# Performance work log

Measured on AMD Instinct MI355X. Metric: run time of the kernel, lower is better.

Reference implementation:

```python
import jax, jax.numpy as jnp
import numpy as np

N_NODES = 50000
N_EDGES = 1600000
IN_DIM = 6
H = 64


def _sage_conv(x, src, dst, W_l, b_l, W_r, num_nodes):
    """PyG SAGEConv (aggr='mean'): out = lin_l(mean_{j in N(i)} x_j) + lin_r(x_i).
    lin_l has bias, lin_r has no bias (PyG default)."""
    # mean-aggregate neighbor features at destination nodes
    agg = jax.ops.segment_sum(x[src], dst, num_segments=num_nodes)          # [N, d]
    cnt = jax.ops.segment_sum(jnp.ones((src.shape[0],), x.dtype), dst,
                              num_segments=num_nodes)                        # [N]
    mean = agg / jnp.maximum(cnt, 1.0)[:, None]
    return mean @ W_l + b_l + x @ W_r


def setup_inputs() -> dict:
    key = jax.random.key(0)
    ks = jax.random.split(key, 8)
    x = jax.random.normal(ks[0], (N_NODES, IN_DIM), dtype=jnp.float32)
    edge_index = jax.random.randint(ks[1], (2, N_EDGES), 0, N_NODES, dtype=jnp.int64)
    # Kaiming-ish scaled params
    def lin(k, fan_in, fan_out):
        return jax.random.normal(k, (fan_in, fan_out), dtype=jnp.float32) / np.sqrt(fan_in)
    return {
        "x": x,
        "edge_index": edge_index,
        "W1_l": lin(ks[2], IN_DIM, H),
        "b1_l": jnp.zeros((H,), jnp.float32),
        "W1_r": lin(ks[3], IN_DIM, H),
        "W2_l": lin(ks[4], H, H),
        "b2_l": jnp.zeros((H,), jnp.float32),
        "W2_r": lin(ks[5], H, H),
    }


def reference(x, edge_index, W1_l, b1_l, W1_r, W2_l, b2_l, W2_r):
    src, dst = edge_index[0], edge_index[1]
    n = x.shape[0]
    z = jax.nn.relu(_sage_conv(x, src, dst, W1_l, b1_l, W1_r, n))  # [N, H]
    z = _sage_conv(z, src, dst, W2_l, b2_l, W2_r, n)               # [N, H]
    return z
```

## Files before the change

kernel.cpp:

```cpp
#include <hip/hip_runtime.h>

#define N_NODES 50000
#define N_EDGES 1600000
#define IN_DIM 6
#define H 64

#define NBUCKET 196
#define NBLK 196
#define EPB 8192
#define BCAP 9216

#define L2PAD 72
#define ZPLANE ((size_t)(N_NODES + 1) * 32)

__device__ __forceinline__ float bf2f(unsigned short u) {
    return __uint_as_float(((unsigned int)u) << 16);
}
__device__ __forceinline__ unsigned short f2bf(float f) {
    unsigned int u = __float_as_uint(f);
    u += 0x7fffu + ((u >> 16) & 1u);
    return (unsigned short)(u >> 16);
}

__global__ __launch_bounds__(512) void scatter_bucketed(
        const int* __restrict__ ei,
        const float* __restrict__ x,
        int* __restrict__ gcur,
        unsigned int* __restrict__ ebin,
        const float* __restrict__ W2l,
        const float* __restrict__ W2r,
        unsigned short* __restrict__ Wlt,
        unsigned short* __restrict__ Wrt,
        unsigned short* __restrict__ z,
        float* __restrict__ xp) {
    int t = threadIdx.x;
    int gid = blockIdx.x * 512 + t;
    if (gid < N_NODES) {
        const float2* xr = (const float2*)(x + (size_t)gid * IN_DIM);
        float2 p0 = xr[0], p1 = xr[1], p2 = xr[2];
        float4* xw = (float4*)(xp + ((size_t)gid << 3));
        xw[0] = make_float4(p0.x, p0.y, p1.x, p1.y);
        xw[1] = make_float4(p2.x, p2.y, 0.f, 0.f);
    }
    if (blockIdx.x == NBLK) {
        for (int i = t; i < H * H; i += 512) {
            int k = i >> 6, f = i & 63;
            Wlt[f * H + k] = f2bf(W2l[i]);
            Wrt[f * H + k] = f2bf(W2r[i]);
        }
        if (t < 64)
            z[(size_t)(t >> 5) * ZPLANE + (size_t)N_NODES * 32 + (t & 31)] = 0;
        return;
    }
    __shared__ unsigned int sedge[EPB];
    __shared__ int hist[NBUCKET];
    __shared__ int cur[NBUCKET];
    for (int i = t; i < NBUCKET; i += 512) hist[i] = 0;
    __syncthreads();
    int e0 = blockIdx.x * EPB;
    int cnt = min(EPB, N_EDGES - e0);
    const int4* s4 = (const int4*)(ei + e0);
    const int4* d4 = (const int4*)(ei + N_EDGES + e0);
    for (int k = t; k * 4 < cnt; k += 512) {
        int4 sv = s4[k];
        int4 dv = d4[k];
        sedge[k * 4 + 0] = ((unsigned)sv.x << 16) | (unsigned)dv.x;
        sedge[k * 4 + 1] = ((unsigned)sv.y << 16) | (unsigned)dv.y;
        sedge[k * 4 + 2] = ((unsigned)sv.z << 16) | (unsigned)dv.z;
        sedge[k * 4 + 3] = ((unsigned)sv.w << 16) | (unsigned)dv.w;
        atomicAdd(&hist[dv.x >> 8], 1);
        atomicAdd(&hist[dv.y >> 8], 1);
        atomicAdd(&hist[dv.z >> 8], 1);
        atomicAdd(&hist[dv.w >> 8], 1);
    }
    __syncthreads();
    for (int i = t; i < NBUCKET; i += 512)
        cur[i] = atomicAdd(&gcur[i], hist[i]);
    __syncthreads();
    for (int k = t; k * 4 < cnt; k += 512) {
#pragma unroll
        for (int j = 0; j < 4; j++) {
            unsigned int p = sedge[k * 4 + j];
            int b = (int)(p & 0xffffu) >> 8;
            int pos = atomicAdd(&cur[b], 1);
            if (pos < BCAP) ebin[(size_t)b * BCAP + pos] = p;
        }
    }
}

__global__ __launch_bounds__(1024) void bucket_layer1(
        const unsigned int* __restrict__ ebin,
        const int* __restrict__ gcur,
        const float* __restrict__ xp,
        const float* __restrict__ W1l,
        const float* __restrict__ b1,
        const float* __restrict__ W1r,
        int2* __restrict__ rowpair,
        unsigned short* __restrict__ esrc,
        unsigned short* __restrict__ z) {
    __shared__ int raw[BCAP];
    __shared__ unsigned short ssrc[BCAP];
    __shared__ int sdeg[256];
    __shared__ int sstart[256];
    __shared__ int scur[256];
    __shared__ int wsum[4];
    __shared__ float sW1l[IN_DIM * H];
    __shared__ float sW1r[IN_DIM * H];
    float* smx   = (float*)raw;
    float* spart = (float*)raw + 4096;

    int t = threadIdx.x;
    int lane = t & 63, w = t >> 6;
    int b = blockIdx.x;
    int base = b << 8;
    int nn = min(256, N_NODES - base);
    int ebase = b * BCAP;
    int cnt = min(gcur[b], BCAP);

    if (t < 256) sdeg[t] = 0;
    if (t < IN_DIM * H) { sW1l[t] = W1l[t]; sW1r[t] = W1r[t]; }
    for (int i = t; i < cnt; i += 1024) raw[i] = (int)ebin[ebase + i];
    __syncthreads();
    for (int i = t; i < cnt; i += 1024) atomicAdd(&sdeg[raw[i] & 0xff], 1);
    __syncthreads();
    int v = 0, s = 0;
    if (t < 256) {
        v = sdeg[t]; s = v;
#pragma unroll
        for (int off = 1; off < 64; off <<= 1) {
            int u = __shfl_up(s, off);
            if (lane >= off) s += u;
        }
        if (lane == 63) wsum[w] = s;
    }
    __syncthreads();
    if (t < 256) {
        int woff = 0;
        for (int k = 0; k < w; k++) woff += wsum[k];
        int excl = s - v + woff;
        sstart[t] = excl;
        scur[t] = excl;
        if (t < nn) rowpair[base + t] = make_int2(ebase + excl, ebase + excl + v);
    }
    __syncthreads();
    for (int i = t; i < cnt; i += 1024) {
        int p = raw[i];
        int pos = atomicAdd(&scur[p & 0xff], 1);
        ssrc[pos] = (unsigned short)((unsigned)p >> 16);
    }
    __syncthreads();
    for (int i = t; i < cnt; i += 1024)
        esrc[ebase + i] = ssrc[i];
    for (int i = t; i < nn * 8; i += 1024) {
        int node = i >> 3, k = i & 7;
        if (k < 6) smx[node * 16 + 6 + k] = xp[(size_t)(base + node) * 8 + k];
    }

    int node = t & 255, q = t >> 8;
    float a0 = 0.f, a1 = 0.f, a2 = 0.f, a3 = 0.f, a4 = 0.f, a5 = 0.f;
    int deg = 0, st = 0;
    if (node < nn) { deg = sdeg[node]; st = sstart[node]; }
    for (int i = st + q; i < st + deg; i += 4) {
        int src = ssrc[i];
        const float4* xs = (const float4*)(xp + ((size_t)src << 3));
        float4 p0 = xs[0], p1 = xs[1];
        a0 += p0.x; a1 += p0.y; a2 += p0.z;
        a3 += p0.w; a4 += p1.x; a5 += p1.y;
    }
    if (q > 0 && node < nn) {
        float* sp = &spart[(q - 1) * (256 * 6) + node * 6];
        sp[0] = a0; sp[1] = a1; sp[2] = a2; sp[3] = a3; sp[4] = a4; sp[5] = a5;
    }
    __syncthreads();
    if (q == 0 && node < nn) {
        float inv = 1.0f / fmaxf((float)deg, 1.0f);
        const float* p1p = &spart[0 * (256 * 6) + node * 6];
        const float* p2p = &spart[1 * (256 * 6) + node * 6];
        const float* p3p = &spart[2 * (256 * 6) + node * 6];
        smx[node * 16 + 0] = (a0 + p1p[0] + p2p[0] + p3p[0]) * inv;
        smx[node * 16 + 1] = (a1 + p1p[1] + p2p[1] + p3p[1]) * inv;
        smx[node * 16 + 2] = (a2 + p1p[2] + p2p[2] + p3p[2]) * inv;
        smx[node * 16 + 3] = (a3 + p1p[3] + p2p[3] + p3p[3]) * inv;
        smx[node * 16 + 4] = (a4 + p1p[4] + p2p[4] + p3p[4]) * inv;
        smx[node * 16 + 5] = (a5 + p1p[5] + p2p[5] + p3p[5]) * inv;
    }
    __syncthreads();

    int feat = t & 63, ng = t >> 6;
    float wl[IN_DIM], wr[IN_DIM];
#pragma unroll
    for (int k = 0; k < IN_DIM; k++) { wl[k] = sW1l[k * H + feat]; wr[k] = sW1r[k * H + feat]; }
    float bias = b1[feat];
    int plane = feat >> 5, f5 = feat & 31;
    unsigned short* zw = z + (size_t)plane * ZPLANE + f5;
    for (int nb = ng; nb < nn; nb += 16) {
        const float4* row = (const float4*)&smx[nb * 16];
        float4 r0 = row[0], r1 = row[1], r2 = row[2];
        float acc = bias;
        acc += r0.x * wl[0] + r0.y * wl[1] + r0.z * wl[2]
             + r0.w * wl[3] + r1.x * wl[4] + r1.y * wl[5];
        acc += r1.z * wr[0] + r1.w * wr[1] + r2.x * wr[2]
             + r2.y * wr[3] + r2.z * wr[4] + r2.w * wr[5];
        zw[(size_t)(base + nb) * 32] = f2bf(fmaxf(acc, 0.0f));
    }
}

__global__ __launch_bounds__(512) void layer2_mfma(
        const unsigned short* __restrict__ zin,
        const int2* __restrict__ rowpair,
        const unsigned short* __restrict__ esrc,
        const unsigned short* __restrict__ Wlt,
        const float* __restrict__ b2,
        const unsigned short* __restrict__ Wrt,
        float* __restrict__ out) {
    typedef short bf16x8 __attribute__((ext_vector_type(8)));
    typedef float f32x4 __attribute__((ext_vector_type(4)));
    __shared__ __attribute__((aligned(16))) unsigned short smean[32 * L2PAD];
    __shared__ __attribute__((aligned(16))) unsigned short szl[32 * L2PAD];
    __shared__ __attribute__((aligned(16))) unsigned short sWl[64 * L2PAD];
    __shared__ __attribute__((aligned(16))) unsigned short sWr[64 * L2PAD];

    int t = threadIdx.x;
    int w = t >> 6, lane = t & 63;
    int g8 = lane >> 3, l8 = lane & 7;
    int n0 = blockIdx.x * 32;

    {
        const ushort4* wl4 = (const ushort4*)Wlt;
        const ushort4* wr4 = (const ushort4*)Wrt;
        for (int qi = t; qi < H * H / 4; qi += 512) {
            int f = qi >> 4, kq = qi & 15;
            *(ushort4*)&sWl[f * L2PAD + kq * 4] = wl4[qi];
            *(ushort4*)&sWr[f * L2PAD + kq * 4] = wr4[qi];
        }
    }

#pragma unroll 1
    for (int pass = 0; pass < 2; pass++) {
        const unsigned short* zp = zin + (size_t)pass * ZPLANE;
        for (int q = 0; q < 4; q++) {
            int ln = w * 4 + q;
            int n = n0 + ln;
            bool valid = (n < N_NODES);
            int r0 = 0, r1 = 0;
            if (valid) { int2 rp = rowpair[n]; r0 = rp.x; r1 = rp.y; }
            float4 acc = make_float4(0.f, 0.f, 0.f, 0.f);
            for (int base = r0; base < r1; base += 64) {
                int ii = base + lane;
                int idx = (ii < r1) ? (int)esrc[ii] : N_NODES;
                int rem = r1 - base;
#pragma unroll
                for (int tt = 0; tt < 4; tt++) {
                    int s = __shfl(idx, tt * 8 + g8);
                    const ushort4* zr = (const ushort4*)(zp + (size_t)s * 32);
                    ushort4 vv = zr[l8];
                    acc.x += bf2f(vv.x); acc.y += bf2f(vv.y);
                    acc.z += bf2f(vv.z); acc.w += bf2f(vv.w);
                }
                if (rem > 32) {
#pragma unroll
                    for (int tt = 4; tt < 8; tt++) {
                        int s = __shfl(idx, tt * 8 + g8);
                        const ushort4* zr = (const ushort4*)(zp + (size_t)s * 32);
                        ushort4 vv = zr[l8];
                        acc.x += bf2f(vv.x); acc.y += bf2f(vv.y);
                        acc.z += bf2f(vv.z); acc.w += bf2f(vv.w);
                    }
                }
            }
#pragma unroll
            for (int off = 8; off < 64; off <<= 1) {
                acc.x += __shfl_xor(acc.x, off);
                acc.y += __shfl_xor(acc.y, off);
                acc.z += __shfl_xor(acc.z, off);
                acc.w += __shfl_xor(acc.w, off);
            }
            float inv = 1.0f / fmaxf((float)(r1 - r0), 1.0f);
            if (g8 == 0) {
                ushort4 mb;
                mb.x = f2bf(acc.x * inv); mb.y = f2bf(acc.y * inv);
                mb.z = f2bf(acc.z * inv); mb.w = f2bf(acc.w * inv);
                *(ushort4*)&smean[ln * L2PAD + pass * 32 + l8 * 4] = mb;
            }
            if (pass == 0) {
                int nz = valid ? n : N_NODES;
                szl[ln * L2PAD + lane] =
                    zin[(size_t)(lane >> 5) * ZPLANE + (size_t)nz * 32 + (lane & 31)];
            }
        }
    }
    __syncthreads();

    int g = lane >> 4, lg = lane & 15;
    int nb = w >> 2, fb = w & 3;
    f32x4 acc = {0.f, 0.f, 0.f, 0.f};
#pragma unroll
    for (int ks = 0; ks < 2; ks++) {
        int ko = ks * 32 + g * 8;
        bf16x8 aM = *(const bf16x8*)&smean[(nb * 16 + lg) * L2PAD + ko];
        bf16x8 aZ = *(const bf16x8*)&szl[(nb * 16 + lg) * L2PAD + ko];
        bf16x8 bL = *(const bf16x8*)&sWl[(fb * 16 + lg) * L2PAD + ko];
        bf16x8 bR = *(const bf16x8*)&sWr[(fb * 16 + lg) * L2PAD + ko];
        acc = __builtin_amdgcn_mfma_f32_16x16x32_bf16(aM, bL, acc, 0, 0, 0);
        acc = __builtin_amdgcn_mfma_f32_16x16x32_bf16(aZ, bR, acc, 0, 0, 0);
    }
    float bias = b2[fb * 16 + lg];
#pragma unroll
    for (int r = 0; r < 4; r++) {
        int node = n0 + nb * 16 + g * 4 + r;
        if (node < N_NODES)
            out[(size_t)node * H + fb * 16 + lg] = acc[r] + bias;
    }
}

extern "C" void kernel_launch(void* const* d_in, const int* in_sizes, int n_in,
                              void* d_out, int out_size, void* d_ws, size_t ws_size,
                              hipStream_t stream) {
    const float* x   = (const float*)d_in[0];
    const int*   ei  = (const int*)d_in[1];
    const float* W1l = (const float*)d_in[2];
    const float* b1  = (const float*)d_in[3];
    const float* W1r = (const float*)d_in[4];
    const float* W2l = (const float*)d_in[5];
    const float* b2  = (const float*)d_in[6];
    const float* W2r = (const float*)d_in[7];
    float* out = (float*)d_out;

    int* gcur = (int*)d_ws;
    int2* rowpair = (int2*)(gcur + 208);
    unsigned int*   ebin = (unsigned int*)(rowpair + N_NODES);
    unsigned short* esrc = (unsigned short*)(ebin + (size_t)NBUCKET * BCAP);
    unsigned short* z    = esrc + (size_t)NBUCKET * BCAP;
    unsigned short* Wlt  = z + 2 * ZPLANE;
    unsigned short* Wrt  = Wlt + H * H;
    float* xp = (float*)(Wrt + H * H);

    hipMemsetAsync(gcur, 0, NBUCKET * sizeof(int), stream);

    scatter_bucketed<<<NBLK + 1, 512, 0, stream>>>(ei, x, gcur, ebin,
                                                   W2l, W2r, Wlt, Wrt, z, xp);
    bucket_layer1<<<NBUCKET, 1024, 0, stream>>>(ebin, gcur, xp, W1l, b1, W1r,
                                                rowpair, esrc, z);
    layer2_mfma<<<(N_NODES + 31) / 32, 512, 0, stream>>>(z, rowpair, esrc,
                                                         Wlt, b2, Wrt, out);
}
```

Before: 154.3 us.

## Replace bucketed edge binning with global per-node degree count, scan, and atomic placement

The two-pass bucket scatter (LDS histogram plus bucket bins, then an in-block counting sort) is replaced by three simpler kernels. One counts per-node in-degree with global atomics, one computes per-bucket exclusive scans into CSR-like row ranges, and one places source indices with per-node global atomics. Layer 1 aggregation is rewritten as a wave-per-node gather with shuffle reduction over 32-node blocks. This removes the intermediate packed edge bin array and the large-LDS layer-1 kernel. In exchange it adds two kernel launches and heavy contended global atomics over 1.6M edges, and the neighbor order within each row becomes nondeterministic.

```diff
diff --git a/kernel.cpp b/kernel.cpp
--- a/kernel.cpp
+++ b/kernel.cpp
@@ -6,12 +6,12 @@
 #define H 64
 
 #define NBUCKET 196
-#define NBLK 196
-#define EPB 8192
 #define BCAP 9216
 
 #define L2PAD 72
 #define ZPLANE ((size_t)(N_NODES + 1) * 32)
+
+#define K1GRID 512
 
 __device__ __forceinline__ float bf2f(unsigned short u) {
     return __uint_as_float(((unsigned int)u) << 16);
@@ -22,11 +22,10 @@
     return (unsigned short)(u >> 16);
 }
 
-__global__ __launch_bounds__(512) void scatter_bucketed(
+__global__ __launch_bounds__(1024) void count_deg(
         const int* __restrict__ ei,
         const float* __restrict__ x,
-        int* __restrict__ gcur,
-        unsigned int* __restrict__ ebin,
+        int* __restrict__ deg,
         const float* __restrict__ W2l,
         const float* __restrict__ W2r,
         unsigned short* __restrict__ Wlt,
@@ -34,155 +33,148 @@
         unsigned short* __restrict__ z,
         float* __restrict__ xp) {
     int t = threadIdx.x;
-    int gid = blockIdx.x * 512 + t;
-    if (gid < N_NODES) {
-        const float2* xr = (const float2*)(x + (size_t)gid * IN_DIM);
+    int tid = blockIdx.x * 1024 + t;
+    if (tid < N_NODES) {
+        const float2* xr = (const float2*)(x + (size_t)tid * IN_DIM);
         float2 p0 = xr[0], p1 = xr[1], p2 = xr[2];
-        float4* xw = (float4*)(xp + ((size_t)gid << 3));
+        float4* xw = (float4*)(xp + ((size_t)tid << 3));
         xw[0] = make_float4(p0.x, p0.y, p1.x, p1.y);
         xw[1] = make_float4(p2.x, p2.y, 0.f, 0.f);
-    }
-    if (blockIdx.x == NBLK) {
-        for (int i = t; i < H * H; i += 512) {
+    } else if (tid == N_NODES) {
+        float4* xw = (float4*)(xp + ((size_t)N_NODES << 3));
+        xw[0] = make_float4(0.f, 0.f, 0.f, 0.f);
+        xw[1] = make_float4(0.f, 0.f, 0.f, 0.f);
+    }
+    if (blockIdx.x == K1GRID - 1) {
+        for (int i = t; i < H * H; i += 1024) {
             int k = i >> 6, f = i & 63;
             Wlt[f * H + k] = f2bf(W2l[i]);
             Wrt[f * H + k] = f2bf(W2r[i]);
         }
         if (t < 64)
             z[(size_t)(t >> 5) * ZPLANE + (size_t)N_NODES * 32 + (t & 31)] = 0;
-        return;
-    }
-    __shared__ unsigned int sedge[EPB];
-    __shared__ int hist[NBUCKET];
-    __shared__ int cur[NBUCKET];
-    for (int i = t; i < NBUCKET; i += 512) hist[i] = 0;
-    __syncthreads();
-    int e0 = blockIdx.x * EPB;
-    int cnt = min(EPB, N_EDGES - e0);
-    const int4* s4 = (const int4*)(ei + e0);
-    const int4* d4 = (const int4*)(ei + N_EDGES + e0);
-    for (int k = t; k * 4 < cnt; k += 512) {
-        int4 sv = s4[k];
-        int4 dv = d4[k];
-        sedge[k * 4 + 0] = ((unsigned)sv.x << 16) | (unsigned)dv.x;
-        sedge[k * 4 + 1] = ((unsigned)sv.y << 16) | (unsigned)dv.y;
-        sedge[k * 4 + 2] = ((unsigned)sv.z << 16) | (unsigned)dv.z;
-        sedge[k * 4 + 3] = ((unsigned)sv.w << 16) | (unsigned)dv.w;
-        atomicAdd(&hist[dv.x >> 8], 1);
-        atomicAdd(&hist[dv.y >> 8], 1);
-        atomicAdd(&hist[dv.z >> 8], 1);
-        atomicAdd(&hist[dv.w >> 8], 1);
-    }
-    __syncthreads();
-    for (int i = t; i < NBUCKET; i += 512)
-        cur[i] = atomicAdd(&gcur[i], hist[i]);
-    __syncthreads();
-    for (int k = t; k * 4 < cnt; k += 512) {
-#pragma unroll
-        for (int j = 0; j < 4; j++) {
-            unsigned int p = sedge[k * 4 + j];
-            int b = (int)(p & 0xffffu) >> 8;
-            int pos = atomicAdd(&cur[b], 1);
-            if (pos < BCAP) ebin[(size_t)b * BCAP + pos] = p;
-        }
-    }
-}
-
-__global__ __launch_bounds__(1024) void bucket_layer1(
-        const unsigned int* __restrict__ ebin,
-        const int* __restrict__ gcur,
-        const float* __restrict__ xp,
-        const float* __restrict__ W1l,
-        const float* __restrict__ b1,
-        const float* __restrict__ W1r,
+    }
+    const int4* d4 = (const int4*)(ei + N_EDGES);
+    if (tid < N_EDGES / 4) {
+        int4 dv = d4[tid];
+        atomicAdd(&deg[dv.x], 1);
+        atomicAdd(&deg[dv.y], 1);
+        atomicAdd(&deg[dv.z], 1);
+        atomicAdd(&deg[dv.w], 1);
+    }
+}
+
+__global__ __launch_bounds__(256) void node_scan(
+        const int* __restrict__ deg,
         int2* __restrict__ rowpair,
-        unsigned short* __restrict__ esrc,
-        unsigned short* __restrict__ z) {
-    __shared__ int raw[BCAP];
-    __shared__ unsigned short ssrc[BCAP];
-    __shared__ int sdeg[256];
-    __shared__ int sstart[256];
-    __shared__ int scur[256];
+        int* __restrict__ cur) {
     __shared__ int wsum[4];
-    __shared__ float sW1l[IN_DIM * H];
-    __shared__ float sW1r[IN_DIM * H];
-    float* smx   = (float*)raw;
-    float* spart = (float*)raw + 4096;
-
     int t = threadIdx.x;
     int lane = t & 63, w = t >> 6;
     int b = blockIdx.x;
     int base = b << 8;
     int nn = min(256, N_NODES - base);
-    int ebase = b * BCAP;
-    int cnt = min(gcur[b], BCAP);
-
-    if (t < 256) sdeg[t] = 0;
+    int v = (t < nn) ? deg[base + t] : 0;
+    int s = v;
+#pragma unroll
+    for (int off = 1; off < 64; off <<= 1) {
+        int u = __shfl_up(s, off);
+        if (lane >= off) s += u;
+    }
+    if (lane == 63) wsum[w] = s;
+    __syncthreads();
+    int woff = 0;
+    for (int k = 0; k < w; k++) woff += wsum[k];
+    int excl = s - v + woff;
+    if (t < nn) {
+        int abs0 = b * BCAP + excl;
+        rowpair[base + t] = make_int2(abs0, abs0 + v);
+        cur[base + t] = abs0;
+    }
+}
+
+__global__ __launch_bounds__(1024) void place_edges(
+        const int* __restrict__ ei,
+        int* __restrict__ cur,
+        unsigned short* __restrict__ esrc) {
+    int tid = blockIdx.x * 1024 + threadIdx.x;
+    if (tid >= N_EDGES / 4) return;
+    const int4* s4 = (const int4*)ei;
+    const int4* d4 = (const int4*)(ei + N_EDGES);
+    int4 sv = s4[tid];
+    int4 dv = d4[tid];
+    int p0 = atomicAdd(&cur[dv.x], 1); esrc[p0] = (unsigned short)sv.x;
+    int p1 = atomicAdd(&cur[dv.y], 1); esrc[p1] = (unsigned short)sv.y;
+    int p2 = atomicAdd(&cur[dv.z], 1); esrc[p2] = (unsigned short)sv.z;
+    int p3 = atomicAdd(&cur[dv.w], 1); esrc[p3] = (unsigned short)sv.w;
+}
+
+__global__ __launch_bounds__(512) void layer1_ns(
+        const float* __restrict__ xp,
+        const int2* __restrict__ rowpair,
+        const unsigned short* __restrict__ esrc,
+        const float* __restrict__ W1l,
+        const float* __restrict__ b1,
+        const float* __restrict__ W1r,
+        unsigned short* __restrict__ z) {
+    __shared__ float smx[32 * 16];
+    __shared__ float sW1l[IN_DIM * H];
+    __shared__ float sW1r[IN_DIM * H];
+
+    int t = threadIdx.x;
+    int w = t >> 6, lane = t & 63;
+    int g16 = lane >> 2, l4 = lane & 3;
+    int n0 = blockIdx.x * 32;
+    int ln0 = w * 4;
+
     if (t < IN_DIM * H) { sW1l[t] = W1l[t]; sW1r[t] = W1r[t]; }
-    for (int i = t; i < cnt; i += 1024) raw[i] = (int)ebin[ebase + i];
-    __syncthreads();
-    for (int i = t; i < cnt; i += 1024) atomicAdd(&sdeg[raw[i] & 0xff], 1);
-    __syncthreads();
-    int v = 0, s = 0;
     if (t < 256) {
-        v = sdeg[t]; s = v;
-#pragma unroll
-        for (int off = 1; off < 64; off <<= 1) {
-            int u = __shfl_up(s, off);
-            if (lane >= off) s += u;
-        }
-        if (lane == 63) wsum[w] = s;
-    }
-    __syncthreads();
-    if (t < 256) {
-        int woff = 0;
-        for (int k = 0; k < w; k++) woff += wsum[k];
-        int excl = s - v + woff;
-        sstart[t] = excl;
-        scur[t] = excl;
-        if (t < nn) rowpair[base + t] = make_int2(ebase + excl, ebase + excl + v);
-    }
-    __syncthreads();
-    for (int i = t; i < cnt; i += 1024) {
-        int p = raw[i];
-        int pos = atomicAdd(&scur[p & 0xff], 1);
-        ssrc[pos] = (unsigned short)((unsigned)p >> 16);
-    }
-    __syncthreads();
-    for (int i = t; i < cnt; i += 1024)
-        esrc[ebase + i] = ssrc[i];
-    for (int i = t; i < nn * 8; i += 1024) {
-        int node = i >> 3, k = i & 7;
-        if (k < 6) smx[node * 16 + 6 + k] = xp[(size_t)(base + node) * 8 + k];
-    }
-
-    int node = t & 255, q = t >> 8;
-    float a0 = 0.f, a1 = 0.f, a2 = 0.f, a3 = 0.f, a4 = 0.f, a5 = 0.f;
-    int deg = 0, st = 0;
-    if (node < nn) { deg = sdeg[node]; st = sstart[node]; }
-    for (int i = st + q; i < st + deg; i += 4) {
-        int src = ssrc[i];
-        const float4* xs = (const float4*)(xp + ((size_t)src << 3));
-        float4 p0 = xs[0], p1 = xs[1];
-        a0 += p0.x; a1 += p0.y; a2 += p0.z;
-        a3 += p0.w; a4 += p1.x; a5 += p1.y;
-    }
-    if (q > 0 && node < nn) {
-        float* sp = &spart[(q - 1) * (256 * 6) + node * 6];
-        sp[0] = a0; sp[1] = a1; sp[2] = a2; sp[3] = a3; sp[4] = a4; sp[5] = a5;
-    }
-    __syncthreads();
-    if (q == 0 && node < nn) {
+        int node = t >> 3, k = t & 7;
+        int n = n0 + node;
+        smx[node * 16 + 8 + k] = (n < N_NODES) ? xp[((size_t)n << 3) + k] : 0.f;
+    }
+
+    for (int j = 0; j < 4; j++) {
+        int n = n0 + ln0 + j;
+        int r0 = 0, r1 = 0;
+        if (n < N_NODES) { int2 rp = rowpair[n]; r0 = rp.x; r1 = rp.y; }
+        int deg = r1 - r0;
+        int ii = r0 + lane;
+        int idx = (ii < r1) ? (int)esrc[ii] : N_NODES;
+        float a0 = 0.f, a1 = 0.f;
+#pragma unroll
+        for (int tt = 0; tt < 4; tt++) {
+            if (tt * 16 >= deg) break;
+            int s = __shfl(idx, tt * 16 + g16);
+            const float2* xr = (const float2*)(xp + ((size_t)s << 3) + l4 * 2);
+            float2 v = xr[0];
+            a0 += v.x; a1 += v.y;
+        }
+        if (deg > 64) {
+            for (int eb = r0 + 64; eb < r1; eb += 64) {
+                int ii2 = eb + lane;
+                int idx2 = (ii2 < r1) ? (int)esrc[ii2] : N_NODES;
+                int rem = r1 - eb;
+#pragma unroll
+                for (int tt = 0; tt < 4; tt++) {
+                    if (tt * 16 >= rem) break;
+                    int s = __shfl(idx2, tt * 16 + g16);
+                    const float2* xr = (const float2*)(xp + ((size_t)s << 3) + l4 * 2);
+                    float2 v = xr[0];
+                    a0 += v.x; a1 += v.y;
+                }
+            }
+        }
+#pragma unroll
+        for (int off = 4; off < 64; off <<= 1) {
+            a0 += __shfl_xor(a0, off);
+            a1 += __shfl_xor(a1, off);
+        }
         float inv = 1.0f / fmaxf((float)deg, 1.0f);
-        const float* p1p = &spart[0 * (256 * 6) + node * 6];
-        const float* p2p = &spart[1 * (256 * 6) + node * 6];
-        const float* p3p = &spart[2 * (256 * 6) + node * 6];
-        smx[node * 16 + 0] = (a0 + p1p[0] + p2p[0] + p3p[0]) * inv;
-        smx[node * 16 + 1] = (a1 + p1p[1] + p2p[1] + p3p[1]) * inv;
-        smx[node * 16 + 2] = (a2 + p1p[2] + p2p[2] + p3p[2]) * inv;
-        smx[node * 16 + 3] = (a3 + p1p[3] + p2p[3] + p3p[3]) * inv;
-        smx[node * 16 + 4] = (a4 + p1p[4] + p2p[4] + p3p[4]) * inv;
-        smx[node * 16 + 5] = (a5 + p1p[5] + p2p[5] + p3p[5]) * inv;
+        if (g16 == 0) {
+            smx[(ln0 + j) * 16 + l4 * 2 + 0] = a0 * inv;
+            smx[(ln0 + j) * 16 + l4 * 2 + 1] = a1 * inv;
+        }
     }
     __syncthreads();
 
@@ -193,15 +185,16 @@
     float bias = b1[feat];
     int plane = feat >> 5, f5 = feat & 31;
     unsigned short* zw = z + (size_t)plane * ZPLANE + f5;
-    for (int nb = ng; nb < nn; nb += 16) {
+    for (int nb = ng; nb < 32; nb += 8) {
+        if (n0 + nb >= N_NODES) break;
         const float4* row = (const float4*)&smx[nb * 16];
-        float4 r0 = row[0], r1 = row[1], r2 = row[2];
+        float4 r0 = row[0], r1 = row[1], r2 = row[2], r3 = row[3];
         float acc = bias;
         acc += r0.x * wl[0] + r0.y * wl[1] + r0.z * wl[2]
              + r0.w * wl[3] + r1.x * wl[4] + r1.y * wl[5];
-        acc += r1.z * wr[0] + r1.w * wr[1] + r2.x * wr[2]
-             + r2.y * wr[3] + r2.z * wr[4] + r2.w * wr[5];
-        zw[(size_t)(base + nb) * 32] = f2bf(fmaxf(acc, 0.0f));
+        acc += r2.x * wr[0] + r2.y * wr[1] + r2.z * wr[2]
+             + r2.w * wr[3] + r3.x * wr[4] + r3.y * wr[5];
+        zw[(size_t)(n0 + nb) * 32] = f2bf(fmaxf(acc, 0.0f));
     }
 }
 
@@ -326,21 +319,22 @@
     const float* W2r = (const float*)d_in[7];
     float* out = (float*)d_out;
 
-    int* gcur = (int*)d_ws;
-    int2* rowpair = (int2*)(gcur + 208);
-    unsigned int*   ebin = (unsigned int*)(rowpair + N_NODES);
-    unsigned short* esrc = (unsigned short*)(ebin + (size_t)NBUCKET * BCAP);
+    int* deg = (int*)d_ws;
+    int* cur = deg + 50016;
+    int2* rowpair = (int2*)(cur + 50016);
+    unsigned short* esrc = (unsigned short*)(rowpair + N_NODES);
     unsigned short* z    = esrc + (size_t)NBUCKET * BCAP;
     unsigned short* Wlt  = z + 2 * ZPLANE;
     unsigned short* Wrt  = Wlt + H * H;
     float* xp = (float*)(Wrt + H * H);
 
-    hipMemsetAsync(gcur, 0, NBUCKET * sizeof(int), stream);
-
-    scatter_bucketed<<<NBLK + 1, 512, 0, stream>>>(ei, x, gcur, ebin,
-                                                   W2l, W2r, Wlt, Wrt, z, xp);
-    bucket_layer1<<<NBUCKET, 1024, 0, stream>>>(ebin, gcur, xp, W1l, b1, W1r,
-                                                rowpair, esrc, z);
+    hipMemsetAsync(deg, 0, 50016 * sizeof(int), stream);
+
+    count_deg<<<K1GRID, 1024, 0, stream>>>(ei, x, deg, W2l, W2r, Wlt, Wrt, z, xp);
+    node_scan<<<NBUCKET, 256, 0, stream>>>(deg, rowpair, cur);
+    place_edges<<<(N_EDGES / 4 + 1023) / 1024, 1024, 0, stream>>>(ei, cur, esrc);
+    layer1_ns<<<(N_NODES + 31) / 32, 512, 0, stream>>>(xp, rowpair, esrc,
+                                                       W1l, b1, W1r, z);
     layer2_mfma<<<(N_NODES + 31) / 32, 512, 0, stream>>>(z, rowpair, esrc,
                                                          Wlt, b2, Wrt, out);
 }
```

Result: slower. 301.8 us (+95.6%).
